# Optimization experiments

Measured on AMD Instinct MI355X. Metric: run time of the kernel, lower is better.

Reference implementation:

```python
import jax, jax.numpy as jnp
import numpy as np

N = 50000      # nodes
E = 800000     # edges
IN = 128       # in_channels
H = 128        # hidden_channels
OUT = 500      # out_channels
EPS = 1e-5


def setup_inputs() -> dict:
    key = jax.random.key(0)
    ks = jax.random.split(key, 8)
    def rn(k, shape, scale=0.05):
        return jax.random.normal(k, shape, jnp.float32) * scale
    return {
        "x": jax.random.normal(ks[0], (N, IN), jnp.float32),
        "edge_index": jax.random.randint(ks[1], (2, E), 0, N, dtype=jnp.int32),
        "W1": rn(ks[2], (IN, H)), "b1": jnp.zeros((H,), jnp.float32),
        "g1": jnp.ones((H,), jnp.float32), "be1": jnp.zeros((H,), jnp.float32),
        "W2": rn(ks[3], (H, 2 * H)), "b2": jnp.zeros((2 * H,), jnp.float32),
        "g2": jnp.ones((2 * H,), jnp.float32), "be2": jnp.zeros((2 * H,), jnp.float32),
        "W3": rn(ks[4], (2 * H, H)), "b3": jnp.zeros((H,), jnp.float32),
        "g3": jnp.ones((H,), jnp.float32), "be3": jnp.zeros((H,), jnp.float32),
        "Wl1": rn(ks[5], (H, H // 2)), "bl1": jnp.zeros((H // 2,), jnp.float32),
        "g4": jnp.ones((H // 2,), jnp.float32), "be4": jnp.zeros((H // 2,), jnp.float32),
        "Wl2": rn(ks[6], (H // 2, OUT)), "bl2": jnp.zeros((OUT,), jnp.float32),
    }


def layer_norm(x, g, b):
    mu = jnp.mean(x, axis=-1, keepdims=True)
    var = jnp.mean(jnp.square(x - mu), axis=-1, keepdims=True)
    return (x - mu) * jax.lax.rsqrt(var + EPS) * g + b


def gcn_conv(x, W, b, src, dst, n):
    # PyG GCNConv: x' = D^{-1/2} (A + I) D^{-1/2} (x W) + b, with self-loops.
    h = x @ W                                   # [N, F]
    ones = jnp.ones(src.shape[0], h.dtype)
    deg = jax.ops.segment_sum(ones, dst, num_segments=n) + 1.0  # +1 self-loop
    dinv = jnp.where(deg > 0, jax.lax.rsqrt(deg), 0.0)          # [N]
    coef = dinv[src] * dinv[dst]                # [E]
    agg = jax.ops.segment_sum(h[src] * coef[:, None], dst, num_segments=n)
    agg = agg + h * jnp.square(dinv)[:, None]   # self-loop messages
    return agg + b


def reference(x, edge_index, W1, b1, g1, be1, W2, b2, g2, be2,
              W3, b3, g3, be3, Wl1, bl1, g4, be4, Wl2, bl2):
    # eval mode: dropout is identity
    src, dst = edge_index[0], edge_index[1]
    n = x.shape[0]
    h = jax.nn.elu(layer_norm(gcn_conv(x, W1, b1, src, dst, n), g1, be1))
    h = jax.nn.elu(layer_norm(gcn_conv(h, W2, b2, src, dst, n), g2, be2))
    h = jax.nn.elu(layer_norm(gcn_conv(h, W3, b3, src, dst, n), g3, be3))
    h = jax.nn.elu(layer_norm(h @ Wl1 + bl1, g4, be4))
    return h @ Wl2 + bl2
```

## Files before the change

### kernel.cpp

```cpp
#include <hip/hip_runtime.h>
#include <cstdint>


#define LN_EPS 1e-5f

typedef __attribute__((ext_vector_type(8))) short bf16x8;
typedef __attribute__((ext_vector_type(4))) float f32x4;

static __device__ __forceinline__ ushort f2bf(float f) {
  union { float f; uint u; } c; c.f = f;
  uint u = c.u;
  return (ushort)((u + 0x7fffu + ((u >> 16) & 1u)) >> 16);
}
static __device__ __forceinline__ float bf2f(ushort h) {
  union { uint u; float f; } c; c.u = (uint)h << 16;
  return c.f;
}


__global__ void deg_kernel(const int* __restrict__ dst, int* __restrict__ deg, int E) {
  int e = blockIdx.x * blockDim.x + threadIdx.x;
  if (e < E) atomicAdd(&deg[dst[e]], 1);
}

__global__ void scan1_kernel(const int* __restrict__ deg, int* __restrict__ excl,
                             int* __restrict__ bsums, float* __restrict__ dinv, int N) {
  __shared__ int s[256];
  int tid = threadIdx.x;
  int i = blockIdx.x * 256 + tid;
  int v = (i < N) ? deg[i] : 0;
  s[tid] = v;
  __syncthreads();
  for (int o = 1; o < 256; o <<= 1) {
    int t = (tid >= o) ? s[tid - o] : 0;
    __syncthreads();
    if (tid >= o) s[tid] += t;
    __syncthreads();
  }
  if (i < N) {
    excl[i] = s[tid] - v;
    dinv[i] = rsqrtf((float)v + 1.0f);
  }
  if (tid == 255) bsums[blockIdx.x] = s[tid];
}

__global__ void scan23_kernel(int* __restrict__ rowptr, int* __restrict__ fill,
                              const int* __restrict__ bsums, int N, int Etotal, int nb) {
  __shared__ int sh[256];
  const int tid = threadIdx.x;
  const int bix = blockIdx.x;
  int v = (tid < bix && tid < nb) ? bsums[tid] : 0;
  sh[tid] = v;
  __syncthreads();
  for (int o = 128; o > 0; o >>= 1) {
    if (tid < o) sh[tid] += sh[tid + o];
    __syncthreads();
  }
  const int off = sh[0];
  int i = bix * 256 + tid;
  if (i < N) {
    int r = rowptr[i] + off;
    rowptr[i] = r;
    fill[i] = r;
  } else if (i == N) {
    rowptr[N] = Etotal;
  }
}

__global__ void fill_kernel(const int* __restrict__ src, const int* __restrict__ dst,
                            int* __restrict__ fill, int* __restrict__ srcs, int E) {
  int e = blockIdx.x * blockDim.x + threadIdx.x;
  if (e >= E) return;
  int idx = atomicAdd(&fill[dst[e]], 1);
  srcs[idx] = src[e];
}


struct WConvArgs {
  const float* w[5];
  ushort* wt[5];
  int K[5], N[5];
  int off[6];
};

__global__ void prep_kernel(WConvArgs a, int total, int* __restrict__ deg, int Nn) {
  int i = blockIdx.x * blockDim.x + threadIdx.x;
  if (i < Nn) deg[i] = 0;
  if (i < 768) a.wt[4][32000 + i] = 0;
  if (i >= total) return;
  int m = 0;
  while (i >= a.off[m + 1]) m++;
  int j = i - a.off[m];
  int k = j / a.N[m], n = j - k * a.N[m];
  a.wt[m][(size_t)n * a.K[m] + k] = f2bf(a.w[m][j]);
}

#define TBM 128
#define TBN 128
#define TBK 32
#define LDK 40

template <int AF32>
__global__ __launch_bounds__(256, 2) void mfma_gemm_kernel(
    const void* __restrict__ A, const ushort* __restrict__ Bt,
    const float* __restrict__ bias, ushort* __restrict__ Cout,
    int M, int N, int K) {
  __shared__ ushort As[TBM][LDK];
  __shared__ ushort Bs[TBN][LDK];
  const int tid = threadIdx.x;
  const int lane = tid & 63;
  const int w = tid >> 6;
  const int wm = w & 1, wn = w >> 1;
  const int quad = lane >> 4, l16 = lane & 15;
  const int rowBase = blockIdx.y * TBM;
  const int colBase = blockIdx.x * TBN;

  f32x4 acc[4][4] = {};
  const int lr = tid >> 2;
  const int lk = (tid & 3) * 8;

  for (int k0 = 0; k0 < K; k0 += TBK) {
#pragma unroll
    for (int h = 0; h < 2; h++) {
      int r = lr + h * 64;
      int grow = rowBase + r;
      if (AF32) {
        const float* Af = (const float*)A;
        float4 v0 = make_float4(0.f, 0.f, 0.f, 0.f), v1 = v0;
        if (grow < M) {
          const float* ap = Af + (size_t)grow * K + k0 + lk;
          v0 = *(const float4*)ap;
          v1 = *(const float4*)(ap + 4);
        }
        uint4 wv;
        wv.x = (uint)f2bf(v0.x) | ((uint)f2bf(v0.y) << 16);
        wv.y = (uint)f2bf(v0.z) | ((uint)f2bf(v0.w) << 16);
        wv.z = (uint)f2bf(v1.x) | ((uint)f2bf(v1.y) << 16);
        wv.w = (uint)f2bf(v1.z) | ((uint)f2bf(v1.w) << 16);
        *(uint4*)&As[r][lk] = wv;
      } else {
        const ushort* Ab = (const ushort*)A;
        uint4 va = make_uint4(0, 0, 0, 0);
        if (grow < M) va = *(const uint4*)(Ab + (size_t)grow * K + k0 + lk);
        *(uint4*)&As[r][lk] = va;
      }
      int gcol = colBase + r;
      uint4 vb = make_uint4(0, 0, 0, 0);
      if (gcol < N) vb = *(const uint4*)(Bt + (size_t)gcol * K + k0 + lk);
      *(uint4*)&Bs[r][lk] = vb;
    }
    __syncthreads();
    bf16x8 af[4], bfr[4];
#pragma unroll
    for (int i = 0; i < 4; i++) {
      af[i]  = *(const bf16x8*)&As[wm * 64 + i * 16 + l16][quad * 8];
      bfr[i] = *(const bf16x8*)&Bs[wn * 64 + i * 16 + l16][quad * 8];
    }
#pragma unroll
    for (int i = 0; i < 4; i++)
#pragma unroll
      for (int j = 0; j < 4; j++)
        acc[i][j] = __builtin_amdgcn_mfma_f32_16x16x32_bf16(af[i], bfr[j], acc[i][j], 0, 0, 0);
    __syncthreads();
  }
#pragma unroll
  for (int i = 0; i < 4; i++) {
    int row0 = rowBase + wm * 64 + i * 16 + quad * 4;
#pragma unroll
    for (int j = 0; j < 4; j++) {
      int col = colBase + wn * 64 + j * 16 + l16;
      if (col >= N) continue;
      float bv = bias ? bias[col] : 0.f;
#pragma unroll
      for (int r = 0; r < 4; r++) {
        int row = row0 + r;
        if (row >= M) continue;
        Cout[(size_t)row * N + col] = f2bf(acc[i][j][r] + bv);
      }
    }
  }
}

__global__ __launch_bounds__(256, 2) void l4_kernel(
    const ushort* __restrict__ A, const ushort* __restrict__ Bt1,
    const float* __restrict__ bias1, const float* __restrict__ gamma,
    const float* __restrict__ beta, ushort* __restrict__ Hout, int M) {
  __shared__ ushort As[128][LDK];
  __shared__ ushort Bs[64][LDK];
  const int tid = threadIdx.x;
  const int lane = tid & 63;
  const int w = tid >> 6;
  const int wm = w & 1, wn = w >> 1;
  const int quad = lane >> 4, l16 = lane & 15;
  const int rowBase = blockIdx.x * 128;

  f32x4 acc[4][4] = {};
  const int lr = tid >> 2;
  const int lk = (tid & 3) * 8;

  for (int k0 = 0; k0 < 128; k0 += TBK) {
#pragma unroll
    for (int h = 0; h < 2; h++) {
      int r = lr + h * 64;
      int grow = rowBase + r;
      uint4 va = make_uint4(0, 0, 0, 0);
      if (grow < M) va = *(const uint4*)(A + (size_t)grow * 128 + k0 + lk);
      *(uint4*)&As[r][lk] = va;
      if (h == 0) {
        uint4 vb = *(const uint4*)(Bt1 + (size_t)r * 128 + k0 + lk);
        *(uint4*)&Bs[r][lk] = vb;
      }
    }
    __syncthreads();
    if (wn == 0) {
      bf16x8 af[4], bfr[4];
#pragma unroll
      for (int i = 0; i < 4; i++) {
        af[i]  = *(const bf16x8*)&As[wm * 64 + i * 16 + l16][quad * 8];
        bfr[i] = *(const bf16x8*)&Bs[i * 16 + l16][quad * 8];
      }
#pragma unroll
      for (int i = 0; i < 4; i++)
#pragma unroll
        for (int j = 0; j < 4; j++)
          acc[i][j] = __builtin_amdgcn_mfma_f32_16x16x32_bf16(af[i], bfr[j], acc[i][j], 0, 0, 0);
    }
    __syncthreads();
  }

  if (wn != 0) return;
  const int rowB = wm * 64;
#pragma unroll
  for (int i = 0; i < 4; i++) {
#pragma unroll
    for (int r = 0; r < 4; r++) {
      int row = rowB + i * 16 + quad * 4 + r;
      float v[4];
      float s = 0.f;
#pragma unroll
      for (int j = 0; j < 4; j++) {
        v[j] = acc[i][j][r] + bias1[j * 16 + l16];
        s += v[j];
      }
#pragma unroll
      for (int o = 8; o >= 1; o >>= 1) s += __shfl_xor(s, o, 16);
      float mean = s * (1.0f / 64.0f);
      float q = 0.f;
#pragma unroll
      for (int j = 0; j < 4; j++) {
        float d = v[j] - mean;
        q += d * d;
      }
#pragma unroll
      for (int o = 8; o >= 1; o >>= 1) q += __shfl_xor(q, o, 16);
      float rstd = rsqrtf(q * (1.0f / 64.0f) + LN_EPS);
      int grow = rowBase + row;
      if (grow < M) {
#pragma unroll
        for (int j = 0; j < 4; j++) {
          int col = j * 16 + l16;
          float y = (v[j] - mean) * rstd * gamma[col] + beta[col];
          y = (y > 0.f) ? y : expm1f(y);
          Hout[(size_t)grow * 64 + col] = f2bf(y);
        }
      }
    }
  }
}

__global__ __launch_bounds__(256, 4) void l5_kernel(
    const ushort* __restrict__ H, const ushort* __restrict__ Bt2,
    const float* __restrict__ bias2, float* __restrict__ Cout, int M) {
  __shared__ ushort h4s[16][68];
  __shared__ __align__(16) float sout[16][500];
  const int tid = threadIdx.x;
  const int lane = tid & 63;
  const int w = tid >> 6;
  const int quad = lane >> 4, l16 = lane & 15;
  const int rowBase = blockIdx.x * 16;

  if (tid < 128) {
    int r = tid >> 3, c8 = (tid & 7) * 8;
    int grow = rowBase + r;
    uint4 v = make_uint4(0, 0, 0, 0);
    if (grow < M) v = *(const uint4*)(H + (size_t)grow * 64 + c8);
    *(uint4*)&h4s[r][c8] = v;
  }

  bf16x8 breg[8][2];
  float bvreg[8];
#pragma unroll
  for (int c = 0; c < 8; c++) {
    const int bcol = (w * 8 + c) * 16 + l16;
    breg[c][0] = *(const bf16x8*)(Bt2 + (size_t)bcol * 64 + quad * 8);
    breg[c][1] = *(const bf16x8*)(Bt2 + (size_t)bcol * 64 + 32 + quad * 8);
    bvreg[c] = (bcol < 500) ? bias2[bcol] : 0.f;
  }
  __syncthreads();

  bf16x8 a0 = *(const bf16x8*)&h4s[l16][quad * 8];
  bf16x8 a1 = *(const bf16x8*)&h4s[l16][quad * 8 + 32];
#pragma unroll
  for (int c = 0; c < 8; c++) {
    f32x4 pacc = {0.f, 0.f, 0.f, 0.f};
    pacc = __builtin_amdgcn_mfma_f32_16x16x32_bf16(a0, breg[c][0], pacc, 0, 0, 0);
    pacc = __builtin_amdgcn_mfma_f32_16x16x32_bf16(a1, breg[c][1], pacc, 0, 0, 0);
    const int col = (w * 8 + c) * 16 + l16;
    if (col < 500) {
#pragma unroll
      for (int r = 0; r < 4; r++)
        sout[quad * 4 + r][col] = pacc[r] + bvreg[c];
    }
  }
  __syncthreads();

#pragma unroll
  for (int k = 0; k < 8; k++) {
    int idx = k * 256 + tid;
    if (idx < 2000) {
      int r = idx / 125;
      int c4 = idx - r * 125;
      int grow = rowBase + r;
      if (grow < M) {
        float4 v = *(float4*)&sout[r][c4 * 4];
        *(float4*)&Cout[(size_t)grow * 500 + c4 * 4] = v;
      }
    }
  }
}


static __device__ __forceinline__ void acc8(float* a, uint4 v, float c) {
  a[0] += c * bf2f((ushort)(v.x & 0xffffu)); a[1] += c * bf2f((ushort)(v.x >> 16));
  a[2] += c * bf2f((ushort)(v.y & 0xffffu)); a[3] += c * bf2f((ushort)(v.y >> 16));
  a[4] += c * bf2f((ushort)(v.z & 0xffffu)); a[5] += c * bf2f((ushort)(v.z >> 16));
  a[6] += c * bf2f((ushort)(v.w & 0xffffu)); a[7] += c * bf2f((ushort)(v.w >> 16));
}

__global__ __launch_bounds__(256) void agg_kernel(
    const ushort* __restrict__ hb, const int* __restrict__ rowptr,
    const int* __restrict__ srcs, const float* __restrict__ dinv,
    uint* __restrict__ out, int Nn) {
  const int wave = threadIdx.x >> 6;
  const int n = blockIdx.x * 4 + wave;
  if (n >= Nn) return;
  const int lane = threadIdx.x & 63;
  const int g = lane >> 4, l16 = lane & 15;
  const uint4* h4 = (const uint4*)hb;
  const float di = dinv[n];
  float a[8] = {0.f, 0.f, 0.f, 0.f, 0.f, 0.f, 0.f, 0.f};
  if (g == 0) {
    uint4 sv = h4[(size_t)n * 16 + l16];
    acc8(a, sv, di * di);
  }
  int i = rowptr[n] + g;
  const int e = rowptr[n + 1];
  for (; i + 4 < e; i += 8) {
    int s0 = srcs[i], s1 = srcs[i + 4];
    float c0 = dinv[s0] * di, c1 = dinv[s1] * di;
    uint4 v0 = h4[(size_t)s0 * 16 + l16];
    uint4 v1 = h4[(size_t)s1 * 16 + l16];
    acc8(a, v0, c0);
    acc8(a, v1, c1);
  }
  if (i < e) {
    int s = srcs[i];
    float c = dinv[s] * di;
    uint4 v = h4[(size_t)s * 16 + l16];
    acc8(a, v, c);
  }
#pragma unroll
  for (int k = 0; k < 8; k++) {
    a[k] += __shfl_xor(a[k], 16);
    a[k] += __shfl_xor(a[k], 32);
  }
  if (g == 0) {
    uint4 o;
    o.x = (uint)f2bf(a[0]) | ((uint)f2bf(a[1]) << 16);
    o.y = (uint)f2bf(a[2]) | ((uint)f2bf(a[3]) << 16);
    o.z = (uint)f2bf(a[4]) | ((uint)f2bf(a[5]) << 16);
    o.w = (uint)f2bf(a[6]) | ((uint)f2bf(a[7]) << 16);
    ((uint4*)out)[(size_t)n * 16 + l16] = o;
  }
}

__global__ __launch_bounds__(256) void agg_ln_kernel(
    const ushort* __restrict__ hb, const int* __restrict__ rowptr,
    const int* __restrict__ srcs, const float* __restrict__ dinv,
    const float* __restrict__ bias, const float* __restrict__ gamma,
    const float* __restrict__ beta, uint* __restrict__ out, int Nn) {
  const int wave = threadIdx.x >> 6;
  const int n = blockIdx.x * 4 + wave;
  if (n >= Nn) return;
  const int lane = threadIdx.x & 63;
  const int g = lane >> 4, l16 = lane & 15;
  const uint4* h4 = (const uint4*)hb;
  const float di = dinv[n];
  float a[8] = {0.f, 0.f, 0.f, 0.f, 0.f, 0.f, 0.f, 0.f};
  if (g == 0) {
    uint4 sv = h4[(size_t)n * 16 + l16];
    acc8(a, sv, di * di);
    float4 b0 = ((const float4*)bias)[l16 * 2];
    float4 b1 = ((const float4*)bias)[l16 * 2 + 1];
    a[0] += b0.x; a[1] += b0.y; a[2] += b0.z; a[3] += b0.w;
    a[4] += b1.x; a[5] += b1.y; a[6] += b1.z; a[7] += b1.w;
  }
  int i = rowptr[n] + g;
  const int e = rowptr[n + 1];
  for (; i + 4 < e; i += 8) {
    int s0 = srcs[i], s1 = srcs[i + 4];
    float c0 = dinv[s0] * di, c1 = dinv[s1] * di;
    uint4 v0 = h4[(size_t)s0 * 16 + l16];
    uint4 v1 = h4[(size_t)s1 * 16 + l16];
    acc8(a, v0, c0);
    acc8(a, v1, c1);
  }
  if (i < e) {
    int s = srcs[i];
    float c = dinv[s] * di;
    uint4 v = h4[(size_t)s * 16 + l16];
    acc8(a, v, c);
  }
#pragma unroll
  for (int k = 0; k < 8; k++) {
    a[k] += __shfl_xor(a[k], 16);
    a[k] += __shfl_xor(a[k], 32);
  }
  float s = ((a[0] + a[1]) + (a[2] + a[3])) + ((a[4] + a[5]) + (a[6] + a[7]));
  s += __shfl_xor(s, 8);
  s += __shfl_xor(s, 4);
  s += __shfl_xor(s, 2);
  s += __shfl_xor(s, 1);
  float mean = s * (1.0f / 128.0f);
  float q = 0.f;
#pragma unroll
  for (int k = 0; k < 8; k++) {
    float d = a[k] - mean;
    q += d * d;
  }
  q += __shfl_xor(q, 8);
  q += __shfl_xor(q, 4);
  q += __shfl_xor(q, 2);
  q += __shfl_xor(q, 1);
  float rstd = rsqrtf(q * (1.0f / 128.0f) + LN_EPS);
  if (g == 0) {
    float4 g0 = ((const float4*)gamma)[l16 * 2];
    float4 g1 = ((const float4*)gamma)[l16 * 2 + 1];
    float4 e0 = ((const float4*)beta)[l16 * 2];
    float4 e1 = ((const float4*)beta)[l16 * 2 + 1];
    float gv[8] = {g0.x, g0.y, g0.z, g0.w, g1.x, g1.y, g1.z, g1.w};
    float ev[8] = {e0.x, e0.y, e0.z, e0.w, e1.x, e1.y, e1.z, e1.w};
    float y[8];
#pragma unroll
    for (int k = 0; k < 8; k++) {
      float t = (a[k] - mean) * rstd * gv[k] + ev[k];
      y[k] = (t > 0.f) ? t : expm1f(t);
    }
    uint4 o;
    o.x = (uint)f2bf(y[0]) | ((uint)f2bf(y[1]) << 16);
    o.y = (uint)f2bf(y[2]) | ((uint)f2bf(y[3]) << 16);
    o.z = (uint)f2bf(y[4]) | ((uint)f2bf(y[5]) << 16);
    o.w = (uint)f2bf(y[6]) | ((uint)f2bf(y[7]) << 16);
    ((uint4*)out)[(size_t)n * 16 + l16] = o;
  }
}

template <int F, bool IN_BF16>
__global__ __launch_bounds__(F) void ln_elu_kernel(const void* __restrict__ xin,
                                                   const float* __restrict__ g,
                                                   const float* __restrict__ be,
                                                   ushort* __restrict__ out) {
  constexpr int NW = (F + 63) / 64;
  __shared__ float sb[NW];
  const int row = blockIdx.x;
  const int f = threadIdx.x;
  float v;
  if (IN_BF16) v = bf2f(((const ushort*)xin)[(size_t)row * F + f]);
  else         v = ((const float*)xin)[(size_t)row * F + f];
  float s = v;
#pragma unroll
  for (int o = 32; o >= 1; o >>= 1) s += __shfl_xor(s, o);
  float mean;
  if constexpr (NW == 1) {
    mean = s * (1.0f / F);
  } else {
    if ((f & 63) == 0) sb[f >> 6] = s;
    __syncthreads();
    float t = 0.f;
#pragma unroll
    for (int w2 = 0; w2 < NW; w2++) t += sb[w2];
    mean = t * (1.0f / F);
    __syncthreads();
  }
  float d = v - mean;
  float q = d * d;
#pragma unroll
  for (int o = 32; o >= 1; o >>= 1) q += __shfl_xor(q, o);
  float var;
  if constexpr (NW == 1) {
    var = q * (1.0f / F);
  } else {
    if ((f & 63) == 0) sb[f >> 6] = q;
    __syncthreads();
    float t = 0.f;
#pragma unroll
    for (int w2 = 0; w2 < NW; w2++) t += sb[w2];
    var = t * (1.0f / F);
  }
  float y = d * rsqrtf(var + LN_EPS) * g[f] + be[f];
  out[(size_t)row * F + f] = f2bf((y > 0.f) ? y : expm1f(y));
}


extern "C" void kernel_launch(void* const* d_in, const int* in_sizes, int n_in,
                              void* d_out, int out_size, void* d_ws, size_t ws_size,
                              hipStream_t stream) {
  const float* x   = (const float*)d_in[0];
  const int*   ei  = (const int*)d_in[1];
  const float* W1  = (const float*)d_in[2];
  const float* b1  = (const float*)d_in[3];
  const float* g1  = (const float*)d_in[4];
  const float* be1 = (const float*)d_in[5];
  const float* W2  = (const float*)d_in[6];
  const float* b2  = (const float*)d_in[7];
  const float* g2  = (const float*)d_in[8];
  const float* be2 = (const float*)d_in[9];
  const float* W3  = (const float*)d_in[10];
  const float* b3  = (const float*)d_in[11];
  const float* g3  = (const float*)d_in[12];
  const float* be3 = (const float*)d_in[13];
  const float* Wl1 = (const float*)d_in[14];
  const float* bl1 = (const float*)d_in[15];
  const float* g4  = (const float*)d_in[16];
  const float* be4 = (const float*)d_in[17];
  const float* Wl2 = (const float*)d_in[18];
  const float* bl2 = (const float*)d_in[19];

  const int N = in_sizes[0] / 128;
  const int E = in_sizes[1] / 2;
  const int* esrc = ei;
  const int* edst = ei + E;

  char* p = (char*)d_ws;
  ushort* Pb = (ushort*)p;            p += (size_t)N * 256 * 2;
  ushort* Qb = (ushort*)p;            p += (size_t)N * 256 * 2;
  ushort* W1t = (ushort*)p;           p += 128 * 128 * 2;
  ushort* W2t = (ushort*)p;           p += 128 * 256 * 2;
  ushort* W3t = (ushort*)p;           p += 256 * 128 * 2;
  ushort* Wl1t = (ushort*)p;          p += 128 * 64 * 2;
  ushort* Wl2t = (ushort*)p;          p += 64 * 512 * 2;
  int*   srcs  = (int*)p;             p += (size_t)E * 4;
  int*   deg   = (int*)p;             p += (size_t)N * 4;
  float* dinv  = (float*)p;           p += (size_t)N * 4;
  int*   rowptr= (int*)p;             p += (size_t)(N + 2) * 4;
  int*   fill  = (int*)p;             p += (size_t)N * 4;
  int*   bsums = (int*)p;             p += 256 * 4;

  const int nb = (N + 255) / 256;
  const int eb = (E + 255) / 256;

  WConvArgs wa;
  wa.w[0] = W1;  wa.wt[0] = W1t;  wa.K[0] = 128; wa.N[0] = 128;
  wa.w[1] = W2;  wa.wt[1] = W2t;  wa.K[1] = 128; wa.N[1] = 256;
  wa.w[2] = W3;  wa.wt[2] = W3t;  wa.K[2] = 256; wa.N[2] = 128;
  wa.w[3] = Wl1; wa.wt[3] = Wl1t; wa.K[3] = 128; wa.N[3] = 64;
  wa.w[4] = Wl2; wa.wt[4] = Wl2t; wa.K[4] = 64;  wa.N[4] = 500;
  wa.off[0] = 0;
  for (int m = 0; m < 5; m++) wa.off[m + 1] = wa.off[m] + wa.K[m] * wa.N[m];
  int wtotal = wa.off[5];
  int ptotal = wtotal > N ? wtotal : N;
  prep_kernel<<<(ptotal + 255) / 256, 256, 0, stream>>>(wa, wtotal, deg, N);

  deg_kernel<<<eb, 256, 0, stream>>>(edst, deg, E);
  scan1_kernel<<<nb, 256, 0, stream>>>(deg, rowptr, bsums, dinv, N);
  scan23_kernel<<<(N + 256) / 256, 256, 0, stream>>>(rowptr, fill, bsums, N, E, nb);
  fill_kernel<<<eb, 256, 0, stream>>>(esrc, edst, fill, srcs, E);

  const int ab = (N + 3) / 4;
  auto grid_of = [&](int M, int Nn) {
    return dim3((Nn + TBN - 1) / TBN, (M + TBM - 1) / TBM);
  };

  mfma_gemm_kernel<1><<<grid_of(N, 128), 256, 0, stream>>>(
      x, W1t, nullptr, Pb, N, 128, 128);
  agg_ln_kernel<<<ab, 256, 0, stream>>>(Pb, rowptr, srcs, dinv, b1, g1, be1, (uint*)Qb, N);

  agg_kernel<<<ab, 256, 0, stream>>>(Qb, rowptr, srcs, dinv, (uint*)Pb, N);
  mfma_gemm_kernel<0><<<grid_of(N, 256), 256, 0, stream>>>(
      Pb, W2t, b2, Qb, N, 256, 128);
  ln_elu_kernel<256, true><<<N, 256, 0, stream>>>(Qb, g2, be2, Pb);

  mfma_gemm_kernel<0><<<grid_of(N, 128), 256, 0, stream>>>(
      Pb, W3t, nullptr, Qb, N, 128, 256);
  agg_ln_kernel<<<ab, 256, 0, stream>>>(Qb, rowptr, srcs, dinv, b3, g3, be3, (uint*)Pb, N);

  l4_kernel<<<dim3((N + 127) / 128), 256, 0, stream>>>(
      Pb, Wl1t, bl1, g4, be4, Qb, N);

  l5_kernel<<<dim3((N + 15) / 16), 256, 0, stream>>>(
      Qb, Wl2t, bl2, (float*)d_out, N);
}
```

Before: 514.5 us.

## Rewrite l4 GEMM+LN kernel as register-only per-wave 16-row tiles without LDS

The Linear+LayerNorm+ELU kernel no longer stages A and B tiles through shared memory with barriers, a scheme in which half the waves sat idle. Each wave now loads its 16 A rows and the whole 64x128 weight matrix straight into registers and runs the MFMAs without synchronisation. Blocks cover 64 rows, so the grid doubles. The cost is that every wave re-reads the weights from global memory or cache and uses more registers. This kernel is a small part of the whole pipeline.

```diff
diff --git a/kernel.cpp b/kernel.cpp
--- a/kernel.cpp
+++ b/kernel.cpp
@@ -181,88 +181,67 @@
   }
 }
 
-__global__ __launch_bounds__(256, 2) void l4_kernel(
+__global__ __launch_bounds__(256) void l4_kernel(
     const ushort* __restrict__ A, const ushort* __restrict__ Bt1,
     const float* __restrict__ bias1, const float* __restrict__ gamma,
     const float* __restrict__ beta, ushort* __restrict__ Hout, int M) {
-  __shared__ ushort As[128][LDK];
-  __shared__ ushort Bs[64][LDK];
   const int tid = threadIdx.x;
   const int lane = tid & 63;
   const int w = tid >> 6;
-  const int wm = w & 1, wn = w >> 1;
   const int quad = lane >> 4, l16 = lane & 15;
-  const int rowBase = blockIdx.x * 128;
-
-  f32x4 acc[4][4] = {};
-  const int lr = tid >> 2;
-  const int lk = (tid & 3) * 8;
-
-  for (int k0 = 0; k0 < 128; k0 += TBK) {
-#pragma unroll
-    for (int h = 0; h < 2; h++) {
-      int r = lr + h * 64;
-      int grow = rowBase + r;
-      uint4 va = make_uint4(0, 0, 0, 0);
-      if (grow < M) va = *(const uint4*)(A + (size_t)grow * 128 + k0 + lk);
-      *(uint4*)&As[r][lk] = va;
-      if (h == 0) {
-        uint4 vb = *(const uint4*)(Bt1 + (size_t)r * 128 + k0 + lk);
-        *(uint4*)&Bs[r][lk] = vb;
-      }
-    }
-    __syncthreads();
-    if (wn == 0) {
-      bf16x8 af[4], bfr[4];
-#pragma unroll
-      for (int i = 0; i < 4; i++) {
-        af[i]  = *(const bf16x8*)&As[wm * 64 + i * 16 + l16][quad * 8];
-        bfr[i] = *(const bf16x8*)&Bs[i * 16 + l16][quad * 8];
-      }
-#pragma unroll
-      for (int i = 0; i < 4; i++)
-#pragma unroll
-        for (int j = 0; j < 4; j++)
-          acc[i][j] = __builtin_amdgcn_mfma_f32_16x16x32_bf16(af[i], bfr[j], acc[i][j], 0, 0, 0);
-    }
-    __syncthreads();
-  }
-
-  if (wn != 0) return;
-  const int rowB = wm * 64;
-#pragma unroll
-  for (int i = 0; i < 4; i++) {
-#pragma unroll
-    for (int r = 0; r < 4; r++) {
-      int row = rowB + i * 16 + quad * 4 + r;
-      float v[4];
-      float s = 0.f;
+  const int rowBase = blockIdx.x * 64 + w * 16;
+
+  bf16x8 bfr[4][4];
+#pragma unroll
+  for (int j = 0; j < 4; j++)
+#pragma unroll
+    for (int kk = 0; kk < 4; kk++)
+      bfr[j][kk] = *(const bf16x8*)(Bt1 + (size_t)(j * 16 + l16) * 128 + kk * 32 + quad * 8);
+
+  const int arow = rowBase + l16;
+  bf16x8 af[4] = {};
+  if (arow < M) {
+#pragma unroll
+    for (int kk = 0; kk < 4; kk++)
+      af[kk] = *(const bf16x8*)(A + (size_t)arow * 128 + kk * 32 + quad * 8);
+  }
+
+  f32x4 acc[4] = {};
+#pragma unroll
+  for (int j = 0; j < 4; j++)
+#pragma unroll
+    for (int kk = 0; kk < 4; kk++)
+      acc[j] = __builtin_amdgcn_mfma_f32_16x16x32_bf16(af[kk], bfr[j][kk], acc[j], 0, 0, 0);
+
+#pragma unroll
+  for (int r = 0; r < 4; r++) {
+    float v[4];
+    float s = 0.f;
+#pragma unroll
+    for (int j = 0; j < 4; j++) {
+      v[j] = acc[j][r] + bias1[j * 16 + l16];
+      s += v[j];
+    }
+#pragma unroll
+    for (int o = 8; o >= 1; o >>= 1) s += __shfl_xor(s, o, 16);
+    float mean = s * (1.0f / 64.0f);
+    float q = 0.f;
+#pragma unroll
+    for (int j = 0; j < 4; j++) {
+      float d = v[j] - mean;
+      q += d * d;
+    }
+#pragma unroll
+    for (int o = 8; o >= 1; o >>= 1) q += __shfl_xor(q, o, 16);
+    float rstd = rsqrtf(q * (1.0f / 64.0f) + LN_EPS);
+    int grow = rowBase + quad * 4 + r;
+    if (grow < M) {
 #pragma unroll
       for (int j = 0; j < 4; j++) {
-        v[j] = acc[i][j][r] + bias1[j * 16 + l16];
-        s += v[j];
-      }
-#pragma unroll
-      for (int o = 8; o >= 1; o >>= 1) s += __shfl_xor(s, o, 16);
-      float mean = s * (1.0f / 64.0f);
-      float q = 0.f;
-#pragma unroll
-      for (int j = 0; j < 4; j++) {
-        float d = v[j] - mean;
-        q += d * d;
-      }
-#pragma unroll
-      for (int o = 8; o >= 1; o >>= 1) q += __shfl_xor(q, o, 16);
-      float rstd = rsqrtf(q * (1.0f / 64.0f) + LN_EPS);
-      int grow = rowBase + row;
-      if (grow < M) {
-#pragma unroll
-        for (int j = 0; j < 4; j++) {
-          int col = j * 16 + l16;
-          float y = (v[j] - mean) * rstd * gamma[col] + beta[col];
-          y = (y > 0.f) ? y : expm1f(y);
-          Hout[(size_t)grow * 64 + col] = f2bf(y);
-        }
+        int col = j * 16 + l16;
+        float y = (v[j] - mean) * rstd * gamma[col] + beta[col];
+        y = (y > 0.f) ? y : expm1f(y);
+        Hout[(size_t)grow * 64 + col] = f2bf(y);
       }
     }
   }
@@ -594,7 +573,7 @@
       Pb, W3t, nullptr, Qb, N, 128, 256);
   agg_ln_kernel<<<ab, 256, 0, stream>>>(Qb, rowptr, srcs, dinv, b3, g3, be3, (uint*)Pb, N);
 
-  l4_kernel<<<dim3((N + 127) / 128), 256, 0, stream>>>(
+  l4_kernel<<<dim3((N + 63) / 64), 256, 0, stream>>>(
       Pb, Wl1t, bl1, g4, be4, Qb, N);
 
   l5_kernel<<<dim3((N + 15) / 16), 256, 0, stream>>>(
```

Result: no change. 510.7 us (-0.7%).
